# Kernel optimization log

Measured on AMD Instinct MI355X. Metric: run time of the kernel, lower is better.

## Reference

```python
import jax, jax.numpy as jnp
import numpy as np

# module hyperparameters (match init_kwargs)
IN_PLANES = 64
OUT = 64            # out_planes
N_HASHES = 4
CHUNK = 25          # chunk_size
GROUPS = 8
KS = 56             # kernel_size == attended axis length H
GP = OUT // GROUPS  # group_planes = 8
EPS_N = 5e-5        # F.normalize eps
BN_EPS = 1e-5
F_GW, F_GV1, F_GV2 = 0.1, 0.1, 1.0


def l2norm(x, axis):
    # torch F.normalize(p=2, eps=EPS_N)
    n = jnp.sqrt(jnp.sum(x * x, axis=axis, keepdims=True))
    return x / jnp.maximum(n, EPS_N)


def setup_inputs() -> dict:
    key = jax.random.key(0)
    k1, k2, k3, k4 = jax.random.split(key, 4)
    x = jax.random.normal(k1, (2, IN_PLANES, KS, 56), jnp.float32)
    conv_w = jax.random.normal(k2, (OUT * 3 // 2, IN_PLANES), jnp.float32) * np.float32(np.sqrt(1.0 / IN_PLANES))
    bn_gamma = jnp.ones((OUT * 3 // 2,), jnp.float32)
    bn_beta = jnp.zeros((OUT * 3 // 2,), jnp.float32)
    relative = jax.random.normal(k3, (KS, GP * 3 // 2), jnp.float32) * np.float32(np.sqrt(1.0 / GP))
    # LSH random rotations: hash_buckets = min(56//25 + (56//25)%2, 10) = 2 -> hb//2 = 1
    rotations = jax.random.normal(k4, (OUT // 2, N_HASHES, 1), jnp.float32)
    return dict(x=x, conv_w=conv_w, bn_gamma=bn_gamma, bn_beta=bn_beta,
                relative=relative, rotations=rotations)


def reference(x, conv_w, bn_gamma, bn_beta, relative, rotations):
    # width=False: (N,C,H,W) -> (N,W,C,H), flatten batch with W
    N, C, Hax, W = x.shape
    x = jnp.transpose(x, (0, 3, 1, 2)).reshape(N * W, C, Hax)
    B, H = N * W, Hax
    hash_buckets = min(H // CHUNK + (H // CHUNK) % 2, 10)

    # 1x1 conv + eval-mode BatchNorm (running_mean=0, running_var=1)
    qkv = jnp.einsum('oc,bch->boh', conv_w, x)
    qkv = qkv / np.float32(np.sqrt(1.0 + BN_EPS)) * bn_gamma[None, :, None] + bn_beta[None, :, None]
    # NOTE: original uses raw reshape (B,C3,H) -> (B,H,C3), NOT a transpose
    qkv = qkv.reshape(B, H, OUT * 3 // 2)
    w_match = qkv[..., :OUT // 2]   # (B,H,out/2)
    v_match = qkv[..., OUT // 2:]   # (B,H,out)
    w_emb = relative[:, :GP // 2]
    v_emb = relative[:, GP // 2:]

    # LSH hashing (rotations shared across batch)
    rot = jnp.einsum('btf,fhi->bhti', w_match, rotations)
    rot = jnp.concatenate([rot, -rot], axis=-1)           # (B,nh,H,hash_buckets)
    codes = jnp.argmax(rot, axis=-1)
    codes = codes + (jnp.arange(N_HASHES) * hash_buckets)[None, :, None]
    codes = codes.reshape(B, N_HASHES * H)

    indices = jnp.argsort(codes, axis=-1)                 # stable sort into buckets
    undo = jnp.argsort(indices, axis=-1)
    mod = indices % H
    w_s = jnp.take_along_axis(w_match, mod[:, :, None], axis=1)
    v_s = jnp.take_along_axis(v_match, mod[:, :, None], axis=1)

    padding = (CHUNK - H % CHUNK) % CHUNK                 # 19 here
    w_b = w_s.reshape(B, N_HASHES, H, OUT // 2)
    v_b = v_s.reshape(B, N_HASHES, H, OUT)
    if padding:
        w_b = jnp.concatenate([w_b, w_b[:, :, -padding:, :]], axis=2)
        v_b = jnp.concatenate([v_b, v_b[:, :, -padding:, :]], axis=2)
        w_emb = jnp.concatenate([w_emb, w_emb[-padding:, :]], axis=0)
        v_emb = jnp.concatenate([v_emb, v_emb[-padding:, :]], axis=0)
    # raw reshapes, exactly as torch does (groups folded via flat reshape)
    w_b = w_b.reshape(B, GROUPS, N_HASHES, -1, CHUNK, GP // 2)
    v_b = v_b.reshape(B, GROUPS, N_HASHES, -1, CHUNK, GP)
    w_emb = w_emb.reshape(-1, CHUNK, GP // 2)             # (K,25,4)
    v_emb = v_emb.reshape(-1, CHUNK, GP)                  # (K,25,8)
    K = w_emb.shape[0]

    def adj(t):  # look-around over the chunk axis (dim 3), cat on dim 4
        return jnp.concatenate([t, jnp.roll(t, 1, axis=3), jnp.roll(t, -1, axis=3)], axis=4)

    def adj_emb(t):
        return jnp.concatenate([t, jnp.roll(t, 1, axis=0), jnp.roll(t, -1, axis=0)], axis=1)

    w_m = adj(l2norm(w_b, -1))
    v_a = adj(v_b)
    w_e = adj_emb(w_emb)
    v_e = adj_emb(v_emb)

    raw = jnp.einsum('bghkie,bghkje->bghkij', w_b, w_m)            # (B,g,h,K,25,75)
    emb_sc = F_GW * jnp.einsum('bghkie,kje->bghkij', w_b, w_e)
    ss = jnp.concatenate([raw, emb_sc], axis=1)                    # (B,2g,h,K,25,75)
    ss = l2norm(ss, 1).reshape(B, 2, GROUPS, N_HASHES, K, CHUNK, CHUNK * 3).sum(axis=1)

    bs = jax.nn.logsumexp(ss, axis=-1, keepdims=True)
    score = jnp.exp(ss - bs)
    bs = bs.reshape(B, GROUPS, N_HASHES, K * CHUNK)

    r_out = F_GV2 * jnp.einsum('bgukij,bgukje->bgukie', score, v_a)
    r_emb = F_GV1 * jnp.einsum('bgukij,kje->bgukie', score, v_e)
    ret = jnp.concatenate([r_out, r_emb], axis=-1)                 # (B,g,h,K,25,2*gp)
    ret = ret.reshape(B, N_HASHES, K, CHUNK, OUT * 2)              # raw reshape
    ret = ret.reshape(B, OUT * 2, N_HASHES, K, CHUNK)              # raw reshape
    ret = l2norm(ret, 1).reshape(B, N_HASHES, K, CHUNK, OUT, 2).sum(axis=-1)
    bs = l2norm(bs, 1).sum(axis=1)                                 # (B,h,K*25)

    ret = ret.reshape(B, N_HASHES, K * CHUNK, OUT)
    if padding:
        ret = ret[:, :, :-padding, :]
        bs = bs[:, :, :-padding]
    ret = ret.reshape(B, N_HASHES * H, OUT)
    bs = bs.reshape(B, N_HASHES * H)

    ret = jnp.take_along_axis(ret, undo[:, :, None], axis=1)      # unsort
    bs = jnp.take_along_axis(bs, undo, axis=1)
    ret = ret.reshape(B, N_HASHES, H, OUT)
    bs = bs.reshape(B, N_HASHES, H, 1)

    probs = jax.nn.softmax(bs, axis=1)
    ret = jnp.sum(ret * probs, axis=1)                             # (B,H,out)
    ret = ret.reshape(N, W, H, OUT)
    return jnp.transpose(ret, (0, 3, 2, 1))                        # (N,out,H,W)
```

## Files before the change

kernel.cpp:

```cpp
#include <hip/hip_runtime.h>
#include <math.h>


#define EPSN 5e-5f
#define INV_EPSN 20000.0f
#define LOG2E 1.4426950408889634f
#define LN2   0.6931471805599453f

__device__ __forceinline__ float dot4(const float4 a, const float4 b) {
    return a.x * b.x + a.y * b.y + a.z * b.z + a.w * b.w;
}
__device__ __forceinline__ void fma4(float4& a, float s, const float4 v) {
    a.x += s * v.x; a.y += s * v.y; a.z += s * v.z; a.w += s * v.w;
}

__global__ __launch_bounds__(256) void k0_xT(
        const float* __restrict__ x, float* __restrict__ xT) {
    __shared__ float T[64][57];
    const int n = blockIdx.x, h = blockIdx.y, tid = threadIdx.x;
    const float* xb = x + n * 200704 + h * 56;
    #pragma unroll 7
    for (int i = tid; i < 3584; i += 256) {
        int c = i / 56, w = i % 56;
        T[c][w] = xb[c * 3136 + w];
    }
    __syncthreads();
    float* xo = xT + n * 200704 + h * 3584;
    #pragma unroll 7
    for (int i = tid; i < 3584; i += 256) {
        int w = i / 64, c = i % 64;
        xo[w * 64 + c] = T[c][w];
    }
}

__global__ __launch_bounds__(256) void k12_qkv_sort(
        const float* __restrict__ xT, const float* __restrict__ cw,
        const float* __restrict__ gamma, const float* __restrict__ beta,
        const float* __restrict__ rot, float* __restrict__ qkv,
        int* __restrict__ idx_buf) {
    __shared__ float xsT[56 * 68];
    __shared__ float cws[96 * 64];
    __shared__ float wm[56 * 32];
    __shared__ float rl[128];
    __shared__ float gs[96], bt[96];
    __shared__ int code[224];
    __shared__ int srt[224];
    const int b = blockIdx.x, n = b / 56, w = b % 56, tid = threadIdx.x;
    const float* xTb = xT + n * 200704 + w * 64;
    #pragma unroll 4
    for (int i = tid; i < 896; i += 256) {
        int h = i / 16, cq = i % 16;
        *(float4*)&xsT[h * 68 + cq * 4] =
            *(const float4*)&xTb[h * 3584 + cq * 4];
    }
    #pragma unroll 8
    for (int i = tid; i < 6144; i += 256) cws[i] = cw[i];
    if (tid < 128) rl[tid] = rot[tid];
    if (tid < 96) { gs[tid] = gamma[tid]; bt[tid] = beta[tid]; }
    __syncthreads();
    const float inv_s = 1.0f / sqrtf(1.0f + 1.0e-5f);
    for (int tl = tid; tl < 672; tl += 256) {
        int oq = tl / 28, hp = tl % 28;
        int o0 = oq * 4, h0 = hp * 2;
        float s00 = 0.f, s01 = 0.f, s10 = 0.f, s11 = 0.f;
        float s20 = 0.f, s21 = 0.f, s30 = 0.f, s31 = 0.f;
        #pragma unroll
        for (int cs = 0; cs < 16; ++cs) {
            float4 xv0 = *(const float4*)&xsT[h0 * 68 + cs * 4];
            float4 xv1 = *(const float4*)&xsT[(h0 + 1) * 68 + cs * 4];
            float4 c0 = *(const float4*)&cws[(o0 + 0) * 64 + cs * 4];
            float4 c1 = *(const float4*)&cws[(o0 + 1) * 64 + cs * 4];
            float4 c2 = *(const float4*)&cws[(o0 + 2) * 64 + cs * 4];
            float4 c3 = *(const float4*)&cws[(o0 + 3) * 64 + cs * 4];
            s00 += dot4(xv0, c0); s01 += dot4(xv1, c0);
            s10 += dot4(xv0, c1); s11 += dot4(xv1, c1);
            s20 += dot4(xv0, c2); s21 += dot4(xv1, c2);
            s30 += dot4(xv0, c3); s31 += dot4(xv1, c3);
        }
        #pragma unroll
        for (int qq = 0; qq < 4; ++qq) {
            #pragma unroll
            for (int hh = 0; hh < 2; ++hh) {
                float sv = (qq == 0) ? (hh ? s01 : s00)
                         : (qq == 1) ? (hh ? s11 : s10)
                         : (qq == 2) ? (hh ? s21 : s20)
                                     : (hh ? s31 : s30);
                int o = o0 + qq, h = h0 + hh;
                float val = sv * inv_s * gs[o] + bt[o];
                int j = o * 56 + h;
                qkv[b * 5376 + j] = val;
                int f = j % 96;
                if (f < 32) wm[(j / 96) * 32 + f] = val;
            }
        }
    }
    __syncthreads();
    if (tid < 224) {
        int u = tid / 56, t = tid % 56;
        float s = 0.f;
        #pragma unroll 8
        for (int f = 0; f < 32; ++f) s += wm[t * 32 + f] * rl[f * 4 + u];
        code[tid] = ((s < 0.f) ? 1 : 0) + 2 * u;
    }
    __syncthreads();
    if (tid < 224) {
        int c = code[tid], r = 0;
        #pragma unroll 8
        for (int p = 0; p < 224; ++p) {
            int cp = code[p];
            r += (int)((cp < c) | ((cp == c) & (p < tid)));
        }
        srt[r] = tid;
    }
    __syncthreads();
    if (tid < 224) idx_buf[b * 224 + tid] = srt[tid];
}

__global__ __launch_bounds__(512) void k3_attn(
        const float* __restrict__ qkv, const int* __restrict__ idx_buf,
        const float* __restrict__ rel, float* __restrict__ Rb,
        float* __restrict__ bsb) {
    __shared__ __align__(16) float Wc[8][3][25][4];
    __shared__ __align__(16) float Vb[8][3][25][8];
    __shared__ __align__(16) float WbK[8][25][4];
    __shared__ float DIT[75][25];
    __shared__ __align__(16) float relL[672];
    __shared__ __align__(16) float veL[600];
    __shared__ int ibL[224];
    const int b = blockIdx.x, u = blockIdx.y, k = blockIdx.z;
    const int tid = threadIdx.x;
    const float* q = qkv + b * 5376;

    if (tid < 224) ibL[tid] = idx_buf[b * 224 + tid];
    for (int i2 = tid; i2 < 672; i2 += 512) relL[i2] = rel[i2];
    #pragma unroll 2
    for (int i2 = tid; i2 < 600; i2 += 512) {
        int j = i2 >> 3, c = i2 & 7;
        int roww = (j < 56) ? j : j - 19;
        veL[i2] = rel[roww * 12 + 4 + c];
    }
    __syncthreads();

    #pragma unroll 2
    for (int idx = tid; idx < 600; idx += 512) {
        int i = idx % 25, kk = (idx / 25) % 3, g = idx / 75;
        int p0 = 1200 * g + 300 * u + 100 * kk + 4 * i;
        int h = p0 / 2400, r = p0 % 2400, t = r >> 5, f = r & 31;
        int row = (t < 56) ? t : t - 19;
        int tt = ibL[h * 56 + row] % 56;
        float4 v = *(const float4*)&q[tt * 96 + f];
        if (kk == k) *(float4*)&WbK[g][i][0] = v;
        float ni = fminf(__builtin_amdgcn_rsqf(dot4(v, v)), INV_EPSN);
        v.x *= ni; v.y *= ni; v.z *= ni; v.w *= ni;
        *(float4*)&Wc[g][kk][i][0] = v;
    }
    #pragma unroll 3
    for (int idx = tid; idx < 1200; idx += 512) {
        int half = idx & 1, fr = idx >> 1;
        int i = fr % 25, kk = (fr / 25) % 3, g = fr / 75;
        int p0 = 2400 * g + 600 * u + 200 * kk + 8 * i + 4 * half;
        int h = p0 / 4800, r = p0 % 4800, t = r >> 6, f = r & 63;
        int row = (t < 56) ? t : t - 19;
        int tt = ibL[h * 56 + row] % 56;
        *(float4*)&Vb[g][kk][i][4 * half] = *(const float4*)&q[tt * 96 + 32 + f];
    }
    __syncthreads();

    if (tid < 375) {
        const int i = tid % 25, jg = tid / 25;
        float4 wb8[8];
        #pragma unroll
        for (int g = 0; g < 8; ++g) wb8[g] = *(const float4*)&WbK[g][i][0];
        #pragma unroll
        for (int it = 0; it < 5; ++it) {
            int j = jg * 5 + it;
            int ks = (j >= 25) + (j >= 50), jj = j - ks * 25;
            int roww = (j < 56) ? j : j - 19;
            float4 we = *(const float4*)&relL[roww * 12];
            we.x *= 0.1f; we.y *= 0.1f; we.z *= 0.1f; we.w *= 0.1f;
            float s2 = 0.f;
            #pragma unroll
            for (int g = 0; g < 8; ++g) {
                float4 wcn = *(const float4*)&Wc[g][ks][jj][0];
                float raw = dot4(wb8[g], wcn);
                float emb = dot4(wb8[g], we);
                s2 += raw * raw + emb * emb;
            }
            DIT[j][i] = fminf(__builtin_amdgcn_rsqf(s2), INV_EPSN) * LOG2E;
        }
    }
    __syncthreads();

    #pragma unroll 2
    for (int idx = tid; idx < 600; idx += 512) {
        int i = idx % 25, kk = (idx / 25) % 3, g = idx / 75;
        int tw = kk * 25 + i;
        int roww = (tw < 56) ? tw : tw - 19;
        float4 we = *(const float4*)&relL[roww * 12];
        float4 v = *(const float4*)&Wc[g][kk][i][0];
        v.x += 0.1f * we.x; v.y += 0.1f * we.y;
        v.z += 0.1f * we.z; v.w += 0.1f * we.w;
        *(float4*)&Wc[g][kk][i][0] = v;
    }
    __syncthreads();

    if (tid < 400) {
        const int half = tid & 1, gi = tid >> 1;
        const int g = gi & 7, i = gi >> 3;
        const int co = 4 * half;
        const float4 wbr = *(const float4*)&WbK[g][i][0];
        const float* Wcf = &Wc[g][0][0][0];
        const float* Vbf = &Vb[g][0][0][co];
        const float* vef = &veL[co];
        const float* DIf = &DIT[0][i];
        float se = 0.f;
        float4 av = {0,0,0,0}, ae = {0,0,0,0};
        #pragma unroll 5
        for (int j = 0; j < 75; ++j) {
            float e = __builtin_amdgcn_exp2f(
                dot4(wbr, *(const float4*)&Wcf[j * 4]) * DIf[j * 25]);
            se += e;
            fma4(av, e, *(const float4*)&Vbf[j * 8]);
            fma4(ae, e, *(const float4*)&vef[j * 8]);
        }
        if (half == 0)
            bsb[b * 2400 + g * 300 + u * 75 + k * 25 + i] =
                __builtin_amdgcn_logf(se) * LN2;
        const float rinv = 1.0f / se;
        const float r2 = 0.1f * rinv;
        av.x *= rinv; av.y *= rinv; av.z *= rinv; av.w *= rinv;
        ae.x *= r2;   ae.y *= r2;   ae.z *= r2;   ae.w *= r2;
        float* rp = Rb + b * 38400 + 4800 * g + 1200 * u + 400 * k + 16 * i;
        *(float4*)(rp + co) = av;
        *(float4*)(rp + 8 + co) = ae;
    }
}

__global__ __launch_bounds__(512) void k45_post(
        const float* __restrict__ Rb, const float* __restrict__ bsb,
        const int* __restrict__ idx_buf, float* __restrict__ out) {
    __shared__ float D[300];
    __shared__ float bsn[300];
    __shared__ float retU[224][32];
    __shared__ float bsU[224];
    __shared__ int idxL[224];
    const int b = blockIdx.x, oh = blockIdx.y, tid = threadIdx.x;
    const int n = b / 56, w = b % 56, o0 = oh * 32;
    const float* R = Rb + b * 38400;
    if (tid < 224) idxL[tid] = idx_buf[b * 224 + tid];
    if (tid < 300) {
        float s = 0.f;
        #pragma unroll 16
        for (int c = 0; c < 128; ++c) { float v = R[c * 300 + tid]; s += v * v; }
        D[tid] = fminf(__builtin_amdgcn_rsqf(s), INV_EPSN);
    }
    if (tid < 300) {
        int u = tid / 75, t = tid % 75;
        float s2 = 0.f, sum = 0.f;
        #pragma unroll
        for (int g = 0; g < 8; ++g) {
            float v = bsb[b * 2400 + g * 300 + u * 75 + t];
            s2 += v * v; sum += v;
        }
        bsn[tid] = sum / fmaxf(sqrtf(s2), EPSN);
    }
    __syncthreads();
    if (tid < 224) {
        int u3 = tid / 56, t = tid % 56;
        bsU[idxL[tid]] = bsn[u3 * 75 + t];
    }
    #pragma unroll 4
    for (int idx = tid; idx < 224 * 32; idx += 512) {
        int p = idx >> 5, oc = idx & 31;
        int o = o0 + oc;
        int u3 = p / 56, t = p % 56;
        int k3 = t / 25, i3 = t % 25;
        int q0 = 9600 * u3 + 3200 * k3 + 128 * i3 + 2 * o;
        float2 rv = *(const float2*)&R[q0];
        int r0 = q0 % 300;
        float val = rv.x * D[r0] + rv.y * D[r0 + 1];
        retU[idxL[p]][oc] = val;
    }
    __syncthreads();
    for (int idx = tid; idx < 56 * 32; idx += 512) {
        int h = idx >> 5, oc = idx & 31;
        int o = o0 + oc;
        float b0 = bsU[h], b1 = bsU[56 + h], b2 = bsU[112 + h], b3 = bsU[168 + h];
        float m = fmaxf(fmaxf(b0, b1), fmaxf(b2, b3));
        float e0 = __builtin_amdgcn_exp2f((b0 - m) * LOG2E);
        float e1 = __builtin_amdgcn_exp2f((b1 - m) * LOG2E);
        float e2 = __builtin_amdgcn_exp2f((b2 - m) * LOG2E);
        float e3 = __builtin_amdgcn_exp2f((b3 - m) * LOG2E);
        float ps = e0 + e1 + e2 + e3;
        float val = (retU[h][oc] * e0 + retU[56 + h][oc] * e1 +
                     retU[112 + h][oc] * e2 + retU[168 + h][oc] * e3) / ps;
        out[((n * 64 + o) * 56 + h) * 56 + w] = val;
    }
}

extern "C" void kernel_launch(void* const* d_in, const int* in_sizes, int n_in,
                              void* d_out, int out_size, void* d_ws, size_t ws_size,
                              hipStream_t stream) {
    (void)in_sizes; (void)n_in; (void)out_size; (void)ws_size;
    const float* x     = (const float*)d_in[0];
    const float* cw    = (const float*)d_in[1];
    const float* gamma = (const float*)d_in[2];
    const float* beta  = (const float*)d_in[3];
    const float* rel   = (const float*)d_in[4];
    const float* rot   = (const float*)d_in[5];
    float* ws  = (float*)d_ws;
    float* qkv = ws;
    float* bsb = ws + 602112;
    float* Rb  = ws + 870912;
    float* xT  = Rb;
    int*   idx = (int*)(ws + 5171712);

    k0_xT<<<dim3(2, 56), 256, 0, stream>>>(x, xT);
    k12_qkv_sort<<<112, 256, 0, stream>>>(xT, cw, gamma, beta, rot, qkv, idx);
    k3_attn<<<dim3(112, 4, 3), 512, 0, stream>>>(qkv, idx, rel, Rb, bsb);
    k45_post<<<dim3(112, 2), 512, 0, stream>>>(Rb, bsb, idx, (float*)d_out);
}
```

Before: 142.3 us.

## Merge query-chunk grid dimension into attention kernel loop to reuse staged chunks

The attention kernel no longer launches one block per query chunk k. Each block now loops over all three chunks and reuses the gathered, normalized W/V tiles, which removes the threefold redundant gathering and normalization of the same keys. The raw query is rebuilt from the normalized vector times a stored norm, and the scaled relative embedding is precomputed once into shared memory. The cost is a third as many blocks (448 instead of 1344) doing serial per-chunk work, which lowers parallelism and latency hiding. Reconstructing the raw query from its norm may also introduce small rounding differences.

```diff
diff --git a/kernel.cpp b/kernel.cpp
--- a/kernel.cpp
+++ b/kernel.cpp
@@ -122,17 +122,21 @@
         float* __restrict__ bsb) {
     __shared__ __align__(16) float Wc[8][3][25][4];
     __shared__ __align__(16) float Vb[8][3][25][8];
-    __shared__ __align__(16) float WbK[8][25][4];
-    __shared__ float DIT[75][25];
-    __shared__ __align__(16) float relL[672];
+    __shared__ float nrm[8][3][25];
+    __shared__ float DIT[3][75][25];
+    __shared__ __align__(16) float weL[75][4];
     __shared__ __align__(16) float veL[600];
-    __shared__ int ibL[224];
-    const int b = blockIdx.x, u = blockIdx.y, k = blockIdx.z;
+    int* ibL = (int*)&DIT[0][0][0];
+    const int b = blockIdx.x, u = blockIdx.y;
     const int tid = threadIdx.x;
     const float* q = qkv + b * 5376;
 
     if (tid < 224) ibL[tid] = idx_buf[b * 224 + tid];
-    for (int i2 = tid; i2 < 672; i2 += 512) relL[i2] = rel[i2];
+    for (int i2 = tid; i2 < 300; i2 += 512) {
+        int j = i2 >> 2, c = i2 & 3;
+        int roww = (j < 56) ? j : j - 19;
+        weL[j][c] = 0.1f * rel[roww * 12 + c];
+    }
     #pragma unroll 2
     for (int i2 = tid; i2 < 600; i2 += 512) {
         int j = i2 >> 3, c = i2 & 7;
@@ -149,10 +153,11 @@
         int row = (t < 56) ? t : t - 19;
         int tt = ibL[h * 56 + row] % 56;
         float4 v = *(const float4*)&q[tt * 96 + f];
-        if (kk == k) *(float4*)&WbK[g][i][0] = v;
-        float ni = fminf(__builtin_amdgcn_rsqf(dot4(v, v)), INV_EPSN);
+        float len = fmaxf(sqrtf(dot4(v, v)), EPSN);
+        float ni = 1.0f / len;
         v.x *= ni; v.y *= ni; v.z *= ni; v.w *= ni;
         *(float4*)&Wc[g][kk][i][0] = v;
+        nrm[g][kk][i] = len;
     }
     #pragma unroll 3
     for (int idx = tid; idx < 1200; idx += 512) {
@@ -168,25 +173,31 @@
 
     if (tid < 375) {
         const int i = tid % 25, jg = tid / 25;
-        float4 wb8[8];
         #pragma unroll
-        for (int g = 0; g < 8; ++g) wb8[g] = *(const float4*)&WbK[g][i][0];
-        #pragma unroll
-        for (int it = 0; it < 5; ++it) {
-            int j = jg * 5 + it;
-            int ks = (j >= 25) + (j >= 50), jj = j - ks * 25;
-            int roww = (j < 56) ? j : j - 19;
-            float4 we = *(const float4*)&relL[roww * 12];
-            we.x *= 0.1f; we.y *= 0.1f; we.z *= 0.1f; we.w *= 0.1f;
-            float s2 = 0.f;
+        for (int kq = 0; kq < 3; ++kq) {
+            float4 wb8[8];
             #pragma unroll
             for (int g = 0; g < 8; ++g) {
-                float4 wcn = *(const float4*)&Wc[g][ks][jj][0];
-                float raw = dot4(wb8[g], wcn);
-                float emb = dot4(wb8[g], we);
-                s2 += raw * raw + emb * emb;
-            }
-            DIT[j][i] = fminf(__builtin_amdgcn_rsqf(s2), INV_EPSN) * LOG2E;
+                float4 t4 = *(const float4*)&Wc[g][kq][i][0];
+                float nr = nrm[g][kq][i];
+                wb8[g].x = t4.x * nr; wb8[g].y = t4.y * nr;
+                wb8[g].z = t4.z * nr; wb8[g].w = t4.w * nr;
+            }
+            #pragma unroll
+            for (int it = 0; it < 5; ++it) {
+                int j = jg * 5 + it;
+                int ks = (j >= 25) + (j >= 50), jj = j - ks * 25;
+                float4 we = *(const float4*)&weL[j][0];
+                float s2 = 0.f;
+                #pragma unroll
+                for (int g = 0; g < 8; ++g) {
+                    float4 wcn = *(const float4*)&Wc[g][ks][jj][0];
+                    float raw = dot4(wb8[g], wcn);
+                    float emb = dot4(wb8[g], we);
+                    s2 += raw * raw + emb * emb;
+                }
+                DIT[kq][j][i] = fminf(__builtin_amdgcn_rsqf(s2), INV_EPSN) * LOG2E;
+            }
         }
     }
     __syncthreads();
@@ -194,12 +205,9 @@
     #pragma unroll 2
     for (int idx = tid; idx < 600; idx += 512) {
         int i = idx % 25, kk = (idx / 25) % 3, g = idx / 75;
-        int tw = kk * 25 + i;
-        int roww = (tw < 56) ? tw : tw - 19;
-        float4 we = *(const float4*)&relL[roww * 12];
+        float4 we = *(const float4*)&weL[kk * 25 + i][0];
         float4 v = *(const float4*)&Wc[g][kk][i][0];
-        v.x += 0.1f * we.x; v.y += 0.1f * we.y;
-        v.z += 0.1f * we.z; v.w += 0.1f * we.w;
+        v.x += we.x; v.y += we.y; v.z += we.z; v.w += we.w;
         *(float4*)&Wc[g][kk][i][0] = v;
     }
     __syncthreads();
@@ -208,31 +216,43 @@
         const int half = tid & 1, gi = tid >> 1;
         const int g = gi & 7, i = gi >> 3;
         const int co = 4 * half;
-        const float4 wbr = *(const float4*)&WbK[g][i][0];
         const float* Wcf = &Wc[g][0][0][0];
         const float* Vbf = &Vb[g][0][0][co];
         const float* vef = &veL[co];
-        const float* DIf = &DIT[0][i];
-        float se = 0.f;
-        float4 av = {0,0,0,0}, ae = {0,0,0,0};
-        #pragma unroll 5
-        for (int j = 0; j < 75; ++j) {
-            float e = __builtin_amdgcn_exp2f(
-                dot4(wbr, *(const float4*)&Wcf[j * 4]) * DIf[j * 25]);
-            se += e;
-            fma4(av, e, *(const float4*)&Vbf[j * 8]);
-            fma4(ae, e, *(const float4*)&vef[j * 8]);
-        }
-        if (half == 0)
-            bsb[b * 2400 + g * 300 + u * 75 + k * 25 + i] =
-                __builtin_amdgcn_logf(se) * LN2;
-        const float rinv = 1.0f / se;
-        const float r2 = 0.1f * rinv;
-        av.x *= rinv; av.y *= rinv; av.z *= rinv; av.w *= rinv;
-        ae.x *= r2;   ae.y *= r2;   ae.z *= r2;   ae.w *= r2;
-        float* rp = Rb + b * 38400 + 4800 * g + 1200 * u + 400 * k + 16 * i;
-        *(float4*)(rp + co) = av;
-        *(float4*)(rp + 8 + co) = ae;
+        #pragma unroll 1
+        for (int kq = 0; kq < 3; ++kq) {
+            float4 wbr;
+            {
+                float4 t4 = *(const float4*)&Wc[g][kq][i][0];
+                float4 wei = *(const float4*)&weL[kq * 25 + i][0];
+                float nr = nrm[g][kq][i];
+                wbr.x = (t4.x - wei.x) * nr;
+                wbr.y = (t4.y - wei.y) * nr;
+                wbr.z = (t4.z - wei.z) * nr;
+                wbr.w = (t4.w - wei.w) * nr;
+            }
+            const float* DIf = &DIT[kq][0][i];
+            float se = 0.f;
+            float4 av = {0,0,0,0}, ae = {0,0,0,0};
+            #pragma unroll 5
+            for (int j = 0; j < 75; ++j) {
+                float e = __builtin_amdgcn_exp2f(
+                    dot4(wbr, *(const float4*)&Wcf[j * 4]) * DIf[j * 25]);
+                se += e;
+                fma4(av, e, *(const float4*)&Vbf[j * 8]);
+                fma4(ae, e, *(const float4*)&vef[j * 8]);
+            }
+            if (half == 0)
+                bsb[b * 2400 + g * 300 + u * 75 + kq * 25 + i] =
+                    __builtin_amdgcn_logf(se) * LN2;
+            const float rinv = 1.0f / se;
+            const float r2 = 0.1f * rinv;
+            av.x *= rinv; av.y *= rinv; av.z *= rinv; av.w *= rinv;
+            ae.x *= r2;   ae.y *= r2;   ae.z *= r2;   ae.w *= r2;
+            float* rp = Rb + b * 38400 + 4800 * g + 1200 * u + 400 * kq + 16 * i;
+            *(float4*)(rp + co) = av;
+            *(float4*)(rp + 8 + co) = ae;
+        }
     }
 }
 
@@ -317,6 +337,6 @@
 
     k0_xT<<<dim3(2, 56), 256, 0, stream>>>(x, xT);
     k12_qkv_sort<<<112, 256, 0, stream>>>(xT, cw, gamma, beta, rot, qkv, idx);
-    k3_attn<<<dim3(112, 4, 3), 512, 0, stream>>>(qkv, idx, rel, Rb, bsb);
+    k3_attn<<<dim3(112, 4), 512, 0, stream>>>(qkv, idx, rel, Rb, bsb);
     k45_post<<<dim3(112, 2), 512, 0, stream>>>(Rb, bsb, idx, (float*)d_out);
 }
```

Result: slower. 182.2 us (+28.0%).
